# Kernel optimization log

Hardware: AMD Instinct MI355X
Metric: run time of the kernel (lower is better)

## Reference

```python
import jax, jax.numpy as jnp
import numpy as np

# 32 point clouds of 1024 points each, 16 neighbors, d_in = 32 channels
N, S, B, K, D = 32768, 1024, 32, 16, 32
EPS = 1e-12


def setup_inputs() -> dict:
    key = jax.random.key(0)
    k1, k2, k3 = jax.random.split(key, 3)
    x = jax.random.normal(k1, (N, D), jnp.float32)          # point features
    pos = jax.random.uniform(k2, (N, 3), jnp.float32)        # xyz coords
    batch = jnp.repeat(jnp.arange(B, dtype=jnp.int32), S)    # equal-size segments
    W = jax.random.normal(k3, (10, D), jnp.float32) / np.sqrt(10.0)
    b = jnp.zeros((D,), jnp.float32)
    return {"x": x, "pos": pos, "batch": batch, "W": W, "b": b}


def reference(x, pos, batch, W, b):
    # batch encodes B equal-sized contiguous clouds -> reshape instead of segment ops
    del batch
    p = pos.reshape(B, S, 3)
    f = x.reshape(B, S, D)

    # per-cloud k-NN on squared distances [B, S, S]
    d2 = jnp.sum((p[:, :, None, :] - p[:, None, :, :]) ** 2, axis=-1)
    _, idx = jax.lax.top_k(-d2, K)                            # [B, S, K]

    gather = jax.vmap(lambda a, i: a[i])                      # per-cloud gather
    pos_j = gather(p, idx)                                    # [B, S, K, 3]
    x_j = gather(f, idx)                                      # [B, S, K, D]

    pos_i = jnp.broadcast_to(p[:, :, None, :], pos_j.shape)   # [B, S, K, 3]
    rel = pos_i - pos_j
    dist = jnp.sqrt(jnp.sum(rel * rel, axis=-1, keepdims=True) + EPS)

    # relative spatial encoding: [B, S, K, 10] -> MLP -> [B, S, K, D]
    feats = jnp.concatenate([pos_i, pos_j, rel, dist], axis=-1)
    enc = jax.nn.relu(feats @ W + b)

    out = jnp.concatenate([x_j, enc], axis=-1)                # [B, S, K, 2D]
    return out.reshape(N, K, 2 * D)
```

## Files before the change

kernel.cpp:

```cpp
#include <hip/hip_runtime.h>

typedef unsigned long long u64;
typedef unsigned int u32;

#define B_  32
#define S_  1024
#define K_  16
#define NTK 256
#define QPB 32

__device__ __forceinline__ double pack_key(float d2, int j) {
    return __longlong_as_double(((u64)__float_as_uint(d2) << 32) | (u32)j);
}

__device__ __forceinline__ void ce(double& a, double& b) {
    const double lo = fmin(a, b);
    const double hi = fmax(a, b);
    a = lo; b = hi;
}

__device__ __forceinline__ void sort8(double (&k)[8]) {
    ce(k[0], k[1]); ce(k[2], k[3]); ce(k[4], k[5]); ce(k[6], k[7]);
    ce(k[0], k[2]); ce(k[1], k[3]); ce(k[4], k[6]); ce(k[5], k[7]);
    ce(k[1], k[2]); ce(k[5], k[6]);
    ce(k[0], k[4]); ce(k[1], k[5]); ce(k[2], k[6]); ce(k[3], k[7]);
    ce(k[2], k[4]); ce(k[3], k[5]);
    ce(k[1], k[2]); ce(k[3], k[4]); ce(k[5], k[6]);
}

__device__ __forceinline__ void clean16(double (&k)[16]) {
#pragma unroll
    for (int str = 8; str > 0; str >>= 1) {
#pragma unroll
        for (int t = 0; t < 16; ++t) {
            const int p = t ^ str;
            if (p > t) ce(k[t], k[p]);
        }
    }
}

__global__ __launch_bounds__(NTK, 4)
void knn_fused(const float* __restrict__ pos, const float* __restrict__ x,
               const float* __restrict__ Wm, const float* __restrict__ bv,
               float* __restrict__ out) {
    __shared__ float4 spos[S_];

    const int tid   = threadIdx.x;
    const int cloud = blockIdx.x >> 5;
    const int qbase = (blockIdx.x & 31) * QPB;
    const int base  = cloud * S_;

    for (int r = tid; r < S_; r += NTK) {
        const float* p = pos + (size_t)(base + r) * 3;
        spos[r] = make_float4(p[0], p[1], p[2], 0.0f);
    }
    __syncthreads();

    const int s  = tid & 7;
    const int qi = qbase + (tid >> 3);
    const float4 pi = spos[qi];
    const float pix = pi.x, piy = pi.y, piz = pi.z;

    double key[16];
#pragma unroll
    for (int t = 0; t < 16; ++t)
        key[t] = __longlong_as_double(0x7FEFFFFFFFFFFFFFULL);

    const float4* sp = &spos[s];
    float4 buf[8];
#pragma unroll
    for (int u = 0; u < 8; ++u) buf[u] = sp[8 * u];

    int jlow = s;
    for (int c = 0; c < 16; ++c) {
        double nk[8];
#pragma unroll
        for (int u = 0; u < 8; ++u) {
            const float dx = __fsub_rn(pix, buf[u].x);
            const float dy = __fsub_rn(piy, buf[u].y);
            const float dz = __fsub_rn(piz, buf[u].z);
            const float d2 = __fadd_rn(
                __fadd_rn(__fmul_rn(dx, dx), __fmul_rn(dy, dy)),
                __fmul_rn(dz, dz));
            nk[u] = pack_key(d2, jlow + 8 * u);
        }
        if (c < 15) {
            sp += 64;
#pragma unroll
            for (int u = 0; u < 8; ++u) buf[u] = sp[8 * u];
        }
        jlow += 64;

        sort8(nk);
#pragma unroll
        for (int t = 0; t < 8; ++t)
            key[8 + t] = fmin(key[8 + t], nk[7 - t]);
        clean16(key);
    }

#pragma unroll
    for (int r = 1; r <= 4; r <<= 1) {
        double nk[16];
#pragma unroll
        for (int t = 0; t < 16; ++t)
            nk[t] = __shfl_xor(key[15 - t], r, 64);
#pragma unroll
        for (int t = 0; t < 16; ++t)
            key[t] = fmin(key[t], nk[t]);
        clean16(key);
    }

    const float4* x4 = (const float4*)x;
    const float4* W4 = (const float4*)Wm;
    float4 wcol[10];
#pragma unroll
    for (int m = 0; m < 10; ++m) wcol[m] = W4[m * 8 + s];
    const float4 bb = ((const float4*)bv)[s];

    float4* orow = (float4*)out + (size_t)(base + qi) * (K_ * 16);
#pragma unroll
    for (int k = 0; k < 16; ++k) {
        const int jl = (int)(u32)__double_as_longlong(key[k]);
        const float4 xj = x4[(size_t)(base + jl) * 8 + s];
        const float4 pj = spos[jl];
        const float rx = pix - pj.x, ry = piy - pj.y, rz = piz - pj.z;
        const float dist = sqrtf(rx * rx + ry * ry + rz * rz + 1e-12f);
        const float f[10] = {pix, piy, piz, pj.x, pj.y, pj.z, rx, ry, rz, dist};
        float4 acc = bb;
#pragma unroll
        for (int m = 0; m < 10; ++m) {
            acc.x = fmaf(f[m], wcol[m].x, acc.x);
            acc.y = fmaf(f[m], wcol[m].y, acc.y);
            acc.z = fmaf(f[m], wcol[m].z, acc.z);
            acc.w = fmaf(f[m], wcol[m].w, acc.w);
        }
        acc.x = fmaxf(acc.x, 0.0f);
        acc.y = fmaxf(acc.y, 0.0f);
        acc.z = fmaxf(acc.z, 0.0f);
        acc.w = fmaxf(acc.w, 0.0f);
        orow[k * 16 + s]     = xj;
        orow[k * 16 + 8 + s] = acc;
    }
}

extern "C" void kernel_launch(void* const* d_in, const int* in_sizes, int n_in,
                              void* d_out, int out_size, void* d_ws, size_t ws_size,
                              hipStream_t stream) {
    const float* x   = (const float*)d_in[0];
    const float* pos = (const float*)d_in[1];
    const float* Wm  = (const float*)d_in[3];
    const float* bv  = (const float*)d_in[4];
    float* out = (float*)d_out;

    knn_fused<<<B_ * 32, NTK, 0, stream>>>(pos, x, Wm, bv, out);
}
```

Baseline: 47.32 us.

## Split kNN into float-threshold pass and candidate-collection exact sort

The first pass now keeps a top-16 of float distances only, dropping the packed 64-bit keys, so the sorting network runs on 32-bit min/max. That pass yields a per-lane kth-distance threshold. A second pass recomputes the distances and writes the indices of points at or below the threshold into a shared-memory candidate buffer (capped at 26 per lane). Those candidates are then exact-sorted with packed double keys before the cross-lane merge. The cost is a second distance sweep, one LDS store per point, more shared memory and a lower occupancy hint, and tied candidates beyond the cap could be dropped.

Result: slower. 57.96 us (+22.5%).

```diff
diff --git a/kernel.cpp b/kernel.cpp
--- a/kernel.cpp
+++ b/kernel.cpp
@@ -8,6 +8,33 @@
 #define K_  16
 #define NTK 256
 #define QPB 32
+#define CAP 26
+
+__device__ __forceinline__ void cef(float& a, float& b) {
+    const float lo = fminf(a, b);
+    const float hi = fmaxf(a, b);
+    a = lo; b = hi;
+}
+
+__device__ __forceinline__ void sort8f(float (&k)[8]) {
+    cef(k[0], k[1]); cef(k[2], k[3]); cef(k[4], k[5]); cef(k[6], k[7]);
+    cef(k[0], k[2]); cef(k[1], k[3]); cef(k[4], k[6]); cef(k[5], k[7]);
+    cef(k[1], k[2]); cef(k[5], k[6]);
+    cef(k[0], k[4]); cef(k[1], k[5]); cef(k[2], k[6]); cef(k[3], k[7]);
+    cef(k[2], k[4]); cef(k[3], k[5]);
+    cef(k[1], k[2]); cef(k[3], k[4]); cef(k[5], k[6]);
+}
+
+__device__ __forceinline__ void clean16f(float (&k)[16]) {
+#pragma unroll
+    for (int str = 8; str > 0; str >>= 1) {
+#pragma unroll
+        for (int t = 0; t < 16; ++t) {
+            const int p = t ^ str;
+            if (p > t) cef(k[t], k[p]);
+        }
+    }
+}
 
 __device__ __forceinline__ double pack_key(float d2, int j) {
     return __longlong_as_double(((u64)__float_as_uint(d2) << 32) | (u32)j);
@@ -19,16 +46,24 @@
     a = lo; b = hi;
 }
 
-__device__ __forceinline__ void sort8(double (&k)[8]) {
-    ce(k[0], k[1]); ce(k[2], k[3]); ce(k[4], k[5]); ce(k[6], k[7]);
-    ce(k[0], k[2]); ce(k[1], k[3]); ce(k[4], k[6]); ce(k[5], k[7]);
-    ce(k[1], k[2]); ce(k[5], k[6]);
-    ce(k[0], k[4]); ce(k[1], k[5]); ce(k[2], k[6]); ce(k[3], k[7]);
-    ce(k[2], k[4]); ce(k[3], k[5]);
-    ce(k[1], k[2]); ce(k[3], k[4]); ce(k[5], k[6]);
-}
-
-__device__ __forceinline__ void clean16(double (&k)[16]) {
+__device__ __forceinline__ void sort16d(double (&k)[16]) {
+#pragma unroll
+    for (int size = 2; size <= 16; size <<= 1) {
+#pragma unroll
+        for (int str = size >> 1; str > 0; str >>= 1) {
+#pragma unroll
+            for (int t = 0; t < 16; ++t) {
+                const int p = t ^ str;
+                if (p > t) {
+                    if ((t & size) == 0) ce(k[t], k[p]);
+                    else                 ce(k[p], k[t]);
+                }
+            }
+        }
+    }
+}
+
+__device__ __forceinline__ void clean16d(double (&k)[16]) {
 #pragma unroll
     for (int str = 8; str > 0; str >>= 1) {
 #pragma unroll
@@ -39,11 +74,12 @@
     }
 }
 
-__global__ __launch_bounds__(NTK, 4)
+__global__ __launch_bounds__(NTK, 3)
 void knn_fused(const float* __restrict__ pos, const float* __restrict__ x,
                const float* __restrict__ Wm, const float* __restrict__ bv,
                float* __restrict__ out) {
     __shared__ float4 spos[S_];
+    __shared__ u32    jbuf[(CAP + 1) * NTK];
 
     const int tid   = threadIdx.x;
     const int cloud = blockIdx.x >> 5;
@@ -61,41 +97,94 @@
     const float4 pi = spos[qi];
     const float pix = pi.x, piy = pi.y, piz = pi.z;
 
-    double key[16];
-#pragma unroll
-    for (int t = 0; t < 16; ++t)
-        key[t] = __longlong_as_double(0x7FEFFFFFFFFFFFFFULL);
+    float keyf[16];
+#pragma unroll
+    for (int t = 0; t < 16; ++t) keyf[t] = __int_as_float(0x7F800000);
 
     const float4* sp = &spos[s];
     float4 buf[8];
 #pragma unroll
     for (int u = 0; u < 8; ++u) buf[u] = sp[8 * u];
 
-    int jlow = s;
     for (int c = 0; c < 16; ++c) {
-        double nk[8];
+        float nk[8];
 #pragma unroll
         for (int u = 0; u < 8; ++u) {
             const float dx = __fsub_rn(pix, buf[u].x);
             const float dy = __fsub_rn(piy, buf[u].y);
             const float dz = __fsub_rn(piz, buf[u].z);
-            const float d2 = __fadd_rn(
+            nk[u] = __fadd_rn(
                 __fadd_rn(__fmul_rn(dx, dx), __fmul_rn(dy, dy)),
                 __fmul_rn(dz, dz));
-            nk[u] = pack_key(d2, jlow + 8 * u);
         }
         if (c < 15) {
             sp += 64;
 #pragma unroll
             for (int u = 0; u < 8; ++u) buf[u] = sp[8 * u];
         }
-        jlow += 64;
-
-        sort8(nk);
+        sort8f(nk);
 #pragma unroll
         for (int t = 0; t < 8; ++t)
-            key[8 + t] = fmin(key[8 + t], nk[7 - t]);
-        clean16(key);
+            keyf[8 + t] = fminf(keyf[8 + t], nk[7 - t]);
+        clean16f(keyf);
+    }
+    const float kth = keyf[15];
+
+    u32 fcnt = 0;
+    {
+        const float4* sp2 = &spos[s];
+        float4 rbuf[8];
+#pragma unroll
+        for (int u = 0; u < 8; ++u) rbuf[u] = sp2[8 * u];
+        int jr = s;
+        for (int c = 0; c < 16; ++c) {
+#pragma unroll
+            for (int u = 0; u < 8; ++u) {
+                const float dx = __fsub_rn(pix, rbuf[u].x);
+                const float dy = __fsub_rn(piy, rbuf[u].y);
+                const float dz = __fsub_rn(piz, rbuf[u].z);
+                const float d2 = __fadd_rn(
+                    __fadd_rn(__fmul_rn(dx, dx), __fmul_rn(dy, dy)),
+                    __fmul_rn(dz, dz));
+                const bool adm = (d2 <= kth) && (fcnt < CAP);
+                const u32 row = adm ? fcnt : CAP;
+                jbuf[row * NTK + tid] = (u32)(jr + 8 * u);
+                fcnt += adm ? 1u : 0u;
+            }
+            if (c < 15) {
+                sp2 += 64;
+#pragma unroll
+                for (int u = 0; u < 8; ++u) rbuf[u] = sp2[8 * u];
+            }
+            jr += 64;
+        }
+    }
+
+    double kd[16];
+#pragma unroll
+    for (int t = 0; t < 16; ++t) {
+        const u32 jl = jbuf[t * NTK + tid];
+        const float4 pj = spos[jl];
+        const float dx = __fsub_rn(pix, pj.x);
+        const float dy = __fsub_rn(piy, pj.y);
+        const float dz = __fsub_rn(piz, pj.z);
+        const float d2 = __fadd_rn(
+            __fadd_rn(__fmul_rn(dx, dx), __fmul_rn(dy, dy)),
+            __fmul_rn(dz, dz));
+        kd[t] = pack_key(d2, (int)jl);
+    }
+    sort16d(kd);
+    for (int t = 16; t < (int)fcnt; ++t) {
+        const u32 jl = jbuf[t * NTK + tid];
+        const float4 pj = spos[jl];
+        const float dx = __fsub_rn(pix, pj.x);
+        const float dy = __fsub_rn(piy, pj.y);
+        const float dz = __fsub_rn(piz, pj.z);
+        const float d2 = __fadd_rn(
+            __fadd_rn(__fmul_rn(dx, dx), __fmul_rn(dy, dy)),
+            __fmul_rn(dz, dz));
+        kd[15] = fmin(kd[15], pack_key(d2, (int)jl));
+        clean16d(kd);
     }
 
 #pragma unroll
@@ -103,11 +192,11 @@
         double nk[16];
 #pragma unroll
         for (int t = 0; t < 16; ++t)
-            nk[t] = __shfl_xor(key[15 - t], r, 64);
+            nk[t] = __shfl_xor(kd[15 - t], r, 64);
 #pragma unroll
         for (int t = 0; t < 16; ++t)
-            key[t] = fmin(key[t], nk[t]);
-        clean16(key);
+            kd[t] = fmin(kd[t], nk[t]);
+        clean16d(kd);
     }
 
     const float4* x4 = (const float4*)x;
@@ -120,7 +209,7 @@
     float4* orow = (float4*)out + (size_t)(base + qi) * (K_ * 16);
 #pragma unroll
     for (int k = 0; k < 16; ++k) {
-        const int jl = (int)(u32)__double_as_longlong(key[k]);
+        const int jl = (int)(u32)__double_as_longlong(kd[k]);
         const float4 xj = x4[(size_t)(base + jl) * 8 + s];
         const float4 pj = spos[jl];
         const float rx = pix - pj.x, ry = piy - pj.y, rz = piz - pj.z;
```
